# Kernel optimization log

Measured on AMD Instinct MI355X. Metric: run time of the kernel, lower is better.

Reference implementation:

```python
import jax, jax.numpy as jnp
import numpy as np

N_NODES = 50000


def sage_conv(x, src, dst, Wl, bl, Wr):
    # mean-aggregate neighbor features: message from src -> dst
    msg = x[src]                                            # [E, d]
    agg = jax.ops.segment_sum(msg, dst, num_segments=N_NODES)
    deg = jax.ops.segment_sum(jnp.ones((src.shape[0],), x.dtype), dst,
                              num_segments=N_NODES)
    mean = agg / jnp.clip(deg, 1.0)[:, None]                # [N, d]
    # PyG SAGEConv: lin_l(mean) + lin_r(x); lin_l has bias, lin_r does not
    return mean @ Wl.T + bl + x @ Wr.T


def setup_inputs() -> dict:
    key = jax.random.key(0)
    ks = jax.random.split(key, 10)
    d_in, d_h = 128, 256
    E = 800000
    x = jax.random.normal(ks[0], (N_NODES, d_in), jnp.float32)
    edge_index = jax.random.randint(ks[1], (2, E), 0, N_NODES, jnp.int32)
    s = 0.05
    return {
        "x": x,
        "edge_index": edge_index,
        "W1_l": jax.random.normal(ks[2], (d_h, d_in), jnp.float32) * s,
        "b1": jax.random.normal(ks[3], (d_h,), jnp.float32) * s,
        "W1_r": jax.random.normal(ks[4], (d_h, d_in), jnp.float32) * s,
        "W2_l": jax.random.normal(ks[5], (d_h, d_h), jnp.float32) * s,
        "b2": jax.random.normal(ks[6], (d_h,), jnp.float32) * s,
        "W2_r": jax.random.normal(ks[7], (d_h, d_h), jnp.float32) * s,
        "head_w": jax.random.normal(ks[8], (1, d_h), jnp.float32) * s,
        "head_b": jax.random.normal(ks[9], (1,), jnp.float32) * s,
    }


def reference(x, edge_index, W1_l, b1, W1_r, W2_l, b2, W2_r, head_w, head_b):
    src, dst = edge_index[0], edge_index[1]
    h = jax.nn.relu(sage_conv(x, src, dst, W1_l, b1, W1_r))
    # dropout is identity in eval mode
    h = jax.nn.relu(sage_conv(h, src, dst, W2_l, b2, W2_r))
    out = h @ head_w.T + head_b                              # [N, 1]
    return out[:, 0]                                         # [N]
```

## Files before the change

### kernel.cpp

```cpp
#include <hip/hip_runtime.h>
#include <hip/hip_bf16.h>
#include <hip/hip_fp8.h>

#define D_IN 128
#define D_H  256
#define NBLK 128
#define BSH  7
#define BNODES 128
#define MAXCH 6400

typedef __attribute__((ext_vector_type(8))) short short8;
typedef __attribute__((ext_vector_type(4))) float floatx4;
typedef __attribute__((ext_vector_type(4))) unsigned short ushortx4;

__device__ __forceinline__ unsigned short f2bf(float f) {
    __hip_bfloat16 h = __float2bfloat16(f);
    return *reinterpret_cast<unsigned short*>(&h);
}
__device__ __forceinline__ unsigned char f2fp8(float f) {
    __hip_fp8_e4m3 t(f);
    return (unsigned char)t.__x;
}

__device__ __forceinline__ void excl_scan512(int* vals, int NB, int* part) {
    const int t = threadIdx.x;
    const int i0 = t * 2, i1 = t * 2 + 1;
    int v0 = (i0 < NB) ? vals[i0] : 0;
    int v1 = (i1 < NB) ? vals[i1] : 0;
    part[t] = v0 + v1;
    __syncthreads();
    for (int off = 1; off < 256; off <<= 1) {
        int u = (t >= off) ? part[t - off] : 0;
        __syncthreads();
        part[t] += u;
        __syncthreads();
    }
    const int pre = (t == 0) ? 0 : part[t - 1];
    if (i0 < NB) vals[i0] = pre;
    if (i1 < NB) vals[i1] = pre + v0;
    __syncthreads();
}

__global__ void p1_hist_conv_k(const int* __restrict__ dst, int* __restrict__ cnt2d,
                               int E, int NB,
                               const float* __restrict__ x,
                               unsigned char* __restrict__ xb8, int nx4,
                               const float* __restrict__ w1l, unsigned short* __restrict__ w1lb,
                               const float* __restrict__ w1r, unsigned short* __restrict__ w1rb, int nw14,
                               const float* __restrict__ w2l, unsigned short* __restrict__ w2lb,
                               const float* __restrict__ w2r, unsigned short* __restrict__ w2rb, int nw24) {
    if (blockIdx.x < NBLK) {
        __shared__ int h[512];
        for (int i = threadIdx.x; i < NB; i += 256) h[i] = 0;
        __syncthreads();
        const int CH = (E + NBLK - 1) / NBLK;
        const int e0 = blockIdx.x * CH;
        const int e1 = min(e0 + CH, E);
        for (int e = e0 + threadIdx.x; e < e1; e += 256)
            atomicAdd(&h[dst[e] >> BSH], 1);
        __syncthreads();
        for (int i = threadIdx.x; i < NB; i += 256)
            cnt2d[blockIdx.x * NB + i] = h[i];
        return;
    }
    int i = (blockIdx.x - NBLK) * 256 + threadIdx.x;
    if (i < nx4) {
        float4 v = ((const float4*)x)[i];
        uchar4 c;
        c.x = f2fp8(v.x); c.y = f2fp8(v.y); c.z = f2fp8(v.z); c.w = f2fp8(v.w);
        ((uchar4*)xb8)[i] = c;
        return;
    }
    i -= nx4;
    const float* s; unsigned short* d; int k;
    if (i < nw14) { s = w1l; d = w1lb; k = i; }
    else {
        i -= nw14;
        if (i < nw14) { s = w1r; d = w1rb; k = i; }
        else {
            i -= nw14;
            if (i < nw24) { s = w2l; d = w2lb; k = i; }
            else {
                i -= nw24;
                if (i >= nw24) return;
                s = w2r; d = w2rb; k = i;
            }
        }
    }
    float4 v = ((const float4*)s)[k];
    ushort4 u;
    u.x = f2bf(v.x); u.y = f2bf(v.y); u.z = f2bf(v.z); u.w = f2bf(v.w);
    ((ushort4*)d)[k] = u;
}

__global__ __launch_bounds__(NBLK) void bucket_scan_k(const int* __restrict__ cnt2d,
                                                      int* __restrict__ off2d,
                                                      int* __restrict__ tot, int NB) {
    const int B = blockIdx.x, t = threadIdx.x;
    __shared__ int sc[NBLK];
    __shared__ int orig[NBLK];
    int v = cnt2d[t * NB + B];
    orig[t] = v; sc[t] = v;
    __syncthreads();
    for (int off = 1; off < NBLK; off <<= 1) {
        int u = (t >= off) ? sc[t - off] : 0;
        __syncthreads();
        sc[t] += u;
        __syncthreads();
    }
    off2d[t * NB + B] = sc[t] - orig[t];
    if (t == NBLK - 1) tot[B] = sc[t];
}

__global__ __launch_bounds__(256) void place_k(const int* __restrict__ src,
                                               const int* __restrict__ dst,
                                               const int* __restrict__ cnt2d,
                                               const int* __restrict__ off2d,
                                               const int* __restrict__ tot,
                                               unsigned int* __restrict__ staging,
                                               int E, int NB) {
    __shared__ unsigned int lstage[MAXCH];
    __shared__ int lstart[512], lcur[512], runstart[512];
    __shared__ int part[256];
    const int b = blockIdx.x, tid = threadIdx.x;
    const int CH = (E + NBLK - 1) / NBLK;
    const int e0 = b * CH;
    const int e1 = min(e0 + CH, E);
    const int n = e1 - e0;

    for (int i = tid; i < NB; i += 256) {
        lstart[i] = cnt2d[b * NB + i];
        runstart[i] = tot[i];
    }
    __syncthreads();
    excl_scan512(lstart, NB, part);
    excl_scan512(runstart, NB, part);
    for (int i = tid; i < NB; i += 256) {
        runstart[i] += off2d[b * NB + i];
        lcur[i] = lstart[i];
    }
    __syncthreads();
    for (int e = e0 + tid; e < e1; e += 256) {
        const int d = dst[e];
        const int pos = atomicAdd(&lcur[d >> BSH], 1);
        lstage[pos] = ((unsigned int)d << 16) | (unsigned int)src[e];
    }
    __syncthreads();
    for (int i = tid; i < n; i += 256) {
        const unsigned int u = lstage[i];
        const int bkt = (int)(u >> (16 + BSH));
        staging[runstart[bkt] + (i - lstart[bkt])] = u;
    }
}

__global__ __launch_bounds__(256) void bucket_sort_k(const unsigned int* __restrict__ staging,
                                                     const int* __restrict__ tot,
                                                     int* __restrict__ rp, int* __restrict__ col,
                                                     int M, int NB) {
    const int B = blockIdx.x, tid = threadIdx.x;
    __shared__ int red[256];
    __shared__ int h[BNODES], sc[BNODES], cur[BNODES];
    __shared__ int s0s, s1s;
    int acc = 0;
    for (int i = tid; i < B; i += 256) acc += tot[i];
    red[tid] = acc; __syncthreads();
    for (int off = 128; off > 0; off >>= 1) {
        if (tid < off) red[tid] += red[tid + off];
        __syncthreads();
    }
    if (tid == 0) { s0s = red[0]; s1s = red[0] + tot[B]; }
    if (tid < BNODES) h[tid] = 0;
    __syncthreads();
    const int s0 = s0s, s1 = s1s;
    for (int i = s0 + tid; i < s1; i += 256)
        atomicAdd(&h[(staging[i] >> 16) & (BNODES - 1)], 1);
    __syncthreads();
    if (tid < BNODES) sc[tid] = h[tid];
    __syncthreads();
    for (int off = 1; off < BNODES; off <<= 1) {
        int v = 0;
        if (tid < BNODES && tid >= off) v = sc[tid - off];
        __syncthreads();
        if (tid < BNODES) sc[tid] += v;
        __syncthreads();
    }
    if (tid < BNODES) {
        const int excl = sc[tid] - h[tid];
        const int node = B * BNODES + tid;
        if (node < M) rp[node] = s0 + excl;
        cur[tid] = s0 + excl;
    }
    if (B == NB - 1 && tid == 0) rp[M] = s1;
    __syncthreads();
    for (int i = s0 + tid; i < s1; i += 256) {
        const unsigned int u = staging[i];
        const int pos = atomicAdd(&cur[(u >> 16) & (BNODES - 1)], 1);
        col[pos] = (int)(u & 0xFFFFu);
    }
}

template <int UNP>
__device__ __forceinline__ int agg1_stage(const unsigned char* __restrict__ X8,
                                          const int* __restrict__ col,
                                          int j, int e, int sel, int l32, float* acc) {
    for (; j + 2 * UNP <= e; j += 2 * UNP) {
        int c0[UNP], c1[UNP];
#pragma unroll
        for (int u = 0; u < UNP; ++u) {
            c0[u] = __builtin_nontemporal_load(col + j + 2 * u);
            c1[u] = __builtin_nontemporal_load(col + j + 2 * u + 1);
        }
        unsigned int vals[UNP];
#pragma unroll
        for (int u = 0; u < UNP; ++u) {
            const int cs = sel ? c1[u] : c0[u];
            vals[u] = *(const unsigned int*)(X8 + (size_t)cs * 128 + l32 * 4);
        }
#pragma unroll
        for (int u = 0; u < UNP; ++u) {
            __hip_fp8x4_e4m3 p;
            p.__x = vals[u];
            float4 f = (float4)p;
            acc[0] += f.x; acc[1] += f.y; acc[2] += f.z; acc[3] += f.w;
        }
    }
    return j;
}

__global__ __launch_bounds__(256) void aggregate1_k(
    const unsigned char* __restrict__ X8, const int* __restrict__ col,
    const int* __restrict__ rp, unsigned short* __restrict__ out, int Mnodes) {
    int node = __builtin_amdgcn_readfirstlane((blockIdx.x << 2) + (threadIdx.x >> 6));
    if (node >= Mnodes) return;
    const int lane = threadIdx.x & 63;
    const int sel = lane >> 5;
    const int l32 = lane & 31;
    const int s = rp[node], e = rp[node + 1];
    float acc[4] = {0.f, 0.f, 0.f, 0.f};

    int j = s;
    j = agg1_stage<4>(X8, col, j, e, sel, l32, acc);
    j = agg1_stage<2>(X8, col, j, e, sel, l32, acc);
    j = agg1_stage<1>(X8, col, j, e, sel, l32, acc);
    if (j < e) {
        const int c0 = col[j];
        if (sel == 0) {
            unsigned int v = *(const unsigned int*)(X8 + (size_t)c0 * 128 + l32 * 4);
            __hip_fp8x4_e4m3 p;
            p.__x = v;
            float4 f = (float4)p;
            acc[0] += f.x; acc[1] += f.y; acc[2] += f.z; acc[3] += f.w;
        }
    }
#pragma unroll
    for (int k = 0; k < 4; ++k) acc[k] += __shfl_xor(acc[k], 32, 64);
    const float inv = 1.f / fmaxf((float)(e - s), 1.f);
    if (sel == 0) {
        ushortx4 o;
        o.x = f2bf(acc[0] * inv); o.y = f2bf(acc[1] * inv);
        o.z = f2bf(acc[2] * inv); o.w = f2bf(acc[3] * inv);
        __builtin_nontemporal_store(o, (ushortx4*)(out + (size_t)node * 128 + l32 * 4));
    }
}

template <int UN>
__device__ __forceinline__ int agg_stage_fp8(const unsigned char* __restrict__ X8,
                                             const int* __restrict__ col,
                                             int j, int e, int lane, float* acc) {
    for (; j + UN <= e; j += UN) {
        int cs[UN];
#pragma unroll
        for (int u = 0; u < UN; ++u) cs[u] = __builtin_nontemporal_load(col + j + u);
        unsigned int vals[UN];
#pragma unroll
        for (int u = 0; u < UN; ++u)
            vals[u] = *(const unsigned int*)(X8 + (size_t)cs[u] * 256 + lane * 4);
#pragma unroll
        for (int u = 0; u < UN; ++u) {
            __hip_fp8x4_e4m3 p;
            p.__x = vals[u];
            float4 f = (float4)p;
            acc[0] += f.x; acc[1] += f.y; acc[2] += f.z; acc[3] += f.w;
        }
    }
    return j;
}

__global__ __launch_bounds__(256) void aggregate2_k(
    const unsigned char* __restrict__ X8, const int* __restrict__ col,
    const int* __restrict__ rp, unsigned short* __restrict__ out, int Mnodes) {
    int node = __builtin_amdgcn_readfirstlane((blockIdx.x << 2) + (threadIdx.x >> 6));
    if (node >= Mnodes) return;
    const int lane = threadIdx.x & 63;
    const int s = rp[node], e = rp[node + 1];
    float acc[4] = {0.f, 0.f, 0.f, 0.f};

    int j = s;
    j = agg_stage_fp8<8>(X8, col, j, e, lane, acc);
    j = agg_stage_fp8<4>(X8, col, j, e, lane, acc);
    j = agg_stage_fp8<2>(X8, col, j, e, lane, acc);
    j = agg_stage_fp8<1>(X8, col, j, e, lane, acc);

    const float inv = 1.f / fmaxf((float)(e - s), 1.f);
    ushortx4 o;
    o.x = f2bf(acc[0] * inv); o.y = f2bf(acc[1] * inv);
    o.z = f2bf(acc[2] * inv); o.w = f2bf(acc[3] * inv);
    __builtin_nontemporal_store(o, (ushortx4*)(out + (size_t)node * 256 + lane * 4));
}

template <int K, bool HEAD, bool A2F32>
__global__ __launch_bounds__(256, 4) void gemm_mfma_k(
    const unsigned short* __restrict__ A1, const unsigned short* __restrict__ W1,
    const unsigned short* __restrict__ A2, const float* __restrict__ A2f,
    const unsigned short* __restrict__ W2,
    const float* __restrict__ bias, unsigned short* __restrict__ Hout,
    unsigned char* __restrict__ Hout8,
    const float* __restrict__ hw, const float* __restrict__ hb,
    float* __restrict__ out, int M) {
    __shared__ __align__(16) unsigned short sA[64 * 40];
    __shared__ __align__(16) unsigned short sB[256 * 40];
    __shared__ float head_acc[64];

    constexpr int NCK = K / 32;
    constexpr int NC = 2 * NCK;

    const int tid = threadIdx.x;
    const int wave = tid >> 6;
    const int lane = tid & 63;
    const int c = lane & 15;
    const int q = lane >> 4;
    const int m0 = blockIdx.x * 64;

    if (HEAD && tid < 64) head_acc[tid] = 0.f;

    floatx4 acc[4][4];
#pragma unroll
    for (int mi = 0; mi < 4; ++mi)
#pragma unroll
        for (int ni = 0; ni < 4; ++ni) acc[mi][ni] = (floatx4){0.f, 0.f, 0.f, 0.f};

    const int arow = tid >> 2;
    const int aseg = (tid & 3) * 8;
    const int brow = tid >> 2;
    const int bseg = (tid & 3) * 8;
    int gr = m0 + arow;
    if (gr >= M) gr = M - 1;

    auto loadChunk = [&](int t, short8& a0, short8* b) {
        const unsigned short* Wp = (t >= NCK) ? W2 : W1;
        const int k0 = (t & (NCK - 1)) * 32;
        if (A2F32 && t >= NCK) {
            const float* p = A2f + (size_t)gr * K + k0 + aseg;
            float4 u0 = *(const float4*)(p);
            float4 u1 = *(const float4*)(p + 4);
            a0 = (short8){(short)f2bf(u0.x), (short)f2bf(u0.y), (short)f2bf(u0.z), (short)f2bf(u0.w),
                          (short)f2bf(u1.x), (short)f2bf(u1.y), (short)f2bf(u1.z), (short)f2bf(u1.w)};
        } else {
            const unsigned short* Ap = (t >= NCK) ? A2 : A1;
            a0 = *(const short8*)(Ap + (size_t)gr * K + k0 + aseg);
        }
#pragma unroll
        for (int i = 0; i < 4; ++i)
            b[i] = *(const short8*)(Wp + (size_t)(brow + i * 64) * K + k0 + bseg);
    };

    short8 ca0, cb[4], na0, nb[4];
    loadChunk(0, ca0, cb);

#pragma unroll 1
    for (int t = 0; t < NC; ++t) {
        __syncthreads();
        *(short8*)&sA[arow * 40 + aseg] = ca0;
#pragma unroll
        for (int i = 0; i < 4; ++i)
            *(short8*)&sB[(brow + i * 64) * 40 + bseg] = cb[i];
        if (t + 1 < NC)
            loadChunk(t + 1, na0, nb);
        __syncthreads();

        short8 af[4], bf[4];
#pragma unroll
        for (int mi = 0; mi < 4; ++mi)
            af[mi] = *(const short8*)&sA[(mi * 16 + c) * 40 + q * 8];
#pragma unroll
        for (int ni = 0; ni < 4; ++ni)
            bf[ni] = *(const short8*)&sB[(wave * 64 + ni * 16 + c) * 40 + q * 8];
#pragma unroll
        for (int mi = 0; mi < 4; ++mi)
#pragma unroll
            for (int ni = 0; ni < 4; ++ni)
                acc[mi][ni] = __builtin_amdgcn_mfma_f32_16x16x32_bf16(
                    af[mi], bf[ni], acc[mi][ni], 0, 0, 0);

        ca0 = na0;
#pragma unroll
        for (int i = 0; i < 4; ++i) cb[i] = nb[i];
    }

    if (!HEAD) {
#pragma unroll
        for (int mi = 0; mi < 4; ++mi)
#pragma unroll
            for (int ni = 0; ni < 4; ++ni) {
                const int n = wave * 64 + ni * 16 + c;
                const float bv = bias[n];
#pragma unroll
                for (int reg = 0; reg < 4; ++reg) {
                    const int m = m0 + mi * 16 + q * 4 + reg;
                    if (m < M) {
                        float v = fmaxf(acc[mi][ni][reg] + bv, 0.f);
                        __builtin_nontemporal_store(f2bf(v), &Hout[(size_t)m * 256 + n]);
                        Hout8[(size_t)m * 256 + n] = f2fp8(v);
                    }
                }
            }
    } else {
#pragma unroll
        for (int mi = 0; mi < 4; ++mi) {
            float p[4] = {0.f, 0.f, 0.f, 0.f};
#pragma unroll
            for (int ni = 0; ni < 4; ++ni) {
                const int n = wave * 64 + ni * 16 + c;
                const float bv = bias[n];
                const float hv = hw[n];
#pragma unroll
                for (int reg = 0; reg < 4; ++reg)
                    p[reg] += fmaxf(acc[mi][ni][reg] + bv, 0.f) * hv;
            }
#pragma unroll
            for (int reg = 0; reg < 4; ++reg) {
                float v = p[reg];
                v += __shfl_xor(v, 1, 64);
                v += __shfl_xor(v, 2, 64);
                v += __shfl_xor(v, 4, 64);
                v += __shfl_xor(v, 8, 64);
                if (c == 0) atomicAdd(&head_acc[mi * 16 + q * 4 + reg], v);
            }
        }
        __syncthreads();
        if (tid < 64) {
            const int m = m0 + tid;
            if (m < M) out[m] = head_acc[tid] + hb[0];
        }
    }
}

extern "C" void kernel_launch(void* const* d_in, const int* in_sizes, int n_in,
                              void* d_out, int out_size, void* d_ws, size_t ws_size,
                              hipStream_t stream) {
    const float* x    = (const float*)d_in[0];
    const int*   ei   = (const int*)d_in[1];
    const float* W1l  = (const float*)d_in[2];
    const float* b1   = (const float*)d_in[3];
    const float* W1r  = (const float*)d_in[4];
    const float* W2l  = (const float*)d_in[5];
    const float* b2   = (const float*)d_in[6];
    const float* W2r  = (const float*)d_in[7];
    const float* hw   = (const float*)d_in[8];
    const float* hb   = (const float*)d_in[9];
    float* out = (float*)d_out;

    const int M = in_sizes[0] / D_IN;
    const int E = in_sizes[1] / 2;
    const int* src = ei;
    const int* dst = ei + E;
    const int NB = (M + BNODES - 1) / BNODES;

    size_t off = 0;
    auto alloc = [&](size_t bytes) -> void* {
        void* p = (char*)d_ws + off;
        off += (bytes + 255) & ~(size_t)255;
        return p;
    };
    int* cnt2d = (int*)alloc((size_t)NBLK * NB * 4);
    int* off2d = (int*)alloc((size_t)NBLK * NB * 4);
    int* tot   = (int*)alloc((size_t)NB * 4);
    unsigned int* staging = (unsigned int*)alloc((size_t)E * 4);
    int* rp    = (int*)alloc((size_t)(M + 1) * 4);
    int* col   = (int*)alloc((size_t)E * 4);
    unsigned char*  xb8   = (unsigned char*)alloc((size_t)M * D_IN);
    unsigned short* w1lb  = (unsigned short*)alloc((size_t)D_H * D_IN * 2);
    unsigned short* w1rb  = (unsigned short*)alloc((size_t)D_H * D_IN * 2);
    unsigned short* w2lb  = (unsigned short*)alloc((size_t)D_H * D_H * 2);
    unsigned short* w2rb  = (unsigned short*)alloc((size_t)D_H * D_H * 2);
    unsigned short* mean1 = (unsigned short*)alloc((size_t)M * D_IN * 2);
    unsigned short* h1    = (unsigned short*)alloc((size_t)M * D_H * 2);
    unsigned char*  h8    = (unsigned char*)alloc((size_t)M * D_H);
    unsigned short* mean2 = (unsigned short*)alloc((size_t)M * D_H * 2);

    const int nx4 = (M * D_IN) / 4;
    const int nw14 = (D_H * D_IN) / 4;
    const int nw24 = (D_H * D_H) / 4;
    const int tot4 = nx4 + 2 * nw14 + 2 * nw24;
    const int convblk = (tot4 + 255) / 256;
    p1_hist_conv_k<<<NBLK + convblk, 256, 0, stream>>>(
        dst, cnt2d, E, NB,
        x, xb8, nx4, W1l, w1lb, W1r, w1rb, nw14, W2l, w2lb, W2r, w2rb, nw24);
    bucket_scan_k<<<NB, NBLK, 0, stream>>>(cnt2d, off2d, tot, NB);
    place_k<<<NBLK, 256, 0, stream>>>(src, dst, cnt2d, off2d, tot, staging, E, NB);
    bucket_sort_k<<<NB, 256, 0, stream>>>(staging, tot, rp, col, M, NB);

    const int nblk = (M + 63) / 64;
    const int ablk = (M + 3) / 4;

    aggregate1_k<<<ablk, 256, 0, stream>>>(xb8, col, rp, mean1, M);
    gemm_mfma_k<D_IN, false, true><<<nblk, 256, 0, stream>>>(
        mean1, w1lb, nullptr, x, w1rb, b1, h1, h8, nullptr, nullptr, nullptr, M);

    aggregate2_k<<<ablk, 256, 0, stream>>>(h8, col, rp, mean2, M);
    gemm_mfma_k<D_H, true, false><<<nblk, 256, 0, stream>>>(
        mean2, w2lb, h1, nullptr, w2rb, b2, nullptr, nullptr, hw, hb, out, M);
}
```

Before: 240.3 us.

## Fuse neighbor mean aggregation into GEMM kernels via shared-memory mean tile

Removes the separate aggregate kernels and computes each 64-node tile's neighbor mean directly into shared memory inside the GEMM kernel, which now runs with 512 threads (8 waves, each covering 32 output columns). This avoids writing and re-reading the bf16 mean1/mean2 buffers through global memory and saves two kernel launches. The cost is a serial gather phase at the start of each GEMM block (8 nodes per wave) with no overlap with the MFMA work, a larger shared-memory footprint, and only about 782 blocks to hide gather latency, so occupancy may limit it.

```diff
diff --git a/kernel.cpp b/kernel.cpp
--- a/kernel.cpp
+++ b/kernel.cpp
@@ -227,42 +227,6 @@
     return j;
 }
 
-__global__ __launch_bounds__(256) void aggregate1_k(
-    const unsigned char* __restrict__ X8, const int* __restrict__ col,
-    const int* __restrict__ rp, unsigned short* __restrict__ out, int Mnodes) {
-    int node = __builtin_amdgcn_readfirstlane((blockIdx.x << 2) + (threadIdx.x >> 6));
-    if (node >= Mnodes) return;
-    const int lane = threadIdx.x & 63;
-    const int sel = lane >> 5;
-    const int l32 = lane & 31;
-    const int s = rp[node], e = rp[node + 1];
-    float acc[4] = {0.f, 0.f, 0.f, 0.f};
-
-    int j = s;
-    j = agg1_stage<4>(X8, col, j, e, sel, l32, acc);
-    j = agg1_stage<2>(X8, col, j, e, sel, l32, acc);
-    j = agg1_stage<1>(X8, col, j, e, sel, l32, acc);
-    if (j < e) {
-        const int c0 = col[j];
-        if (sel == 0) {
-            unsigned int v = *(const unsigned int*)(X8 + (size_t)c0 * 128 + l32 * 4);
-            __hip_fp8x4_e4m3 p;
-            p.__x = v;
-            float4 f = (float4)p;
-            acc[0] += f.x; acc[1] += f.y; acc[2] += f.z; acc[3] += f.w;
-        }
-    }
-#pragma unroll
-    for (int k = 0; k < 4; ++k) acc[k] += __shfl_xor(acc[k], 32, 64);
-    const float inv = 1.f / fmaxf((float)(e - s), 1.f);
-    if (sel == 0) {
-        ushortx4 o;
-        o.x = f2bf(acc[0] * inv); o.y = f2bf(acc[1] * inv);
-        o.z = f2bf(acc[2] * inv); o.w = f2bf(acc[3] * inv);
-        __builtin_nontemporal_store(o, (ushortx4*)(out + (size_t)node * 128 + l32 * 4));
-    }
-}
-
 template <int UN>
 __device__ __forceinline__ int agg_stage_fp8(const unsigned char* __restrict__ X8,
                                              const int* __restrict__ col,
@@ -286,39 +250,22 @@
     return j;
 }
 
-__global__ __launch_bounds__(256) void aggregate2_k(
+template <int K, bool HEAD, bool A2F32>
+__global__ __launch_bounds__(512, 4) void gemm_fused_k(
     const unsigned char* __restrict__ X8, const int* __restrict__ col,
-    const int* __restrict__ rp, unsigned short* __restrict__ out, int Mnodes) {
-    int node = __builtin_amdgcn_readfirstlane((blockIdx.x << 2) + (threadIdx.x >> 6));
-    if (node >= Mnodes) return;
-    const int lane = threadIdx.x & 63;
-    const int s = rp[node], e = rp[node + 1];
-    float acc[4] = {0.f, 0.f, 0.f, 0.f};
-
-    int j = s;
-    j = agg_stage_fp8<8>(X8, col, j, e, lane, acc);
-    j = agg_stage_fp8<4>(X8, col, j, e, lane, acc);
-    j = agg_stage_fp8<2>(X8, col, j, e, lane, acc);
-    j = agg_stage_fp8<1>(X8, col, j, e, lane, acc);
-
-    const float inv = 1.f / fmaxf((float)(e - s), 1.f);
-    ushortx4 o;
-    o.x = f2bf(acc[0] * inv); o.y = f2bf(acc[1] * inv);
-    o.z = f2bf(acc[2] * inv); o.w = f2bf(acc[3] * inv);
-    __builtin_nontemporal_store(o, (ushortx4*)(out + (size_t)node * 256 + lane * 4));
-}
-
-template <int K, bool HEAD, bool A2F32>
-__global__ __launch_bounds__(256, 4) void gemm_mfma_k(
-    const unsigned short* __restrict__ A1, const unsigned short* __restrict__ W1,
-    const unsigned short* __restrict__ A2, const float* __restrict__ A2f,
+    const int* __restrict__ rp,
+    const unsigned short* __restrict__ W1,
+    const float* __restrict__ A2f, const unsigned short* __restrict__ A2,
     const unsigned short* __restrict__ W2,
     const float* __restrict__ bias, unsigned short* __restrict__ Hout,
     unsigned char* __restrict__ Hout8,
     const float* __restrict__ hw, const float* __restrict__ hb,
     float* __restrict__ out, int M) {
+
+    constexpr int SMS = K + 8;
+    __shared__ __align__(16) unsigned short sMean[64 * SMS];
+    __shared__ __align__(16) unsigned short sB[256 * 40];
     __shared__ __align__(16) unsigned short sA[64 * 40];
-    __shared__ __align__(16) unsigned short sB[256 * 40];
     __shared__ float head_acc[64];
 
     constexpr int NCK = K / 32;
@@ -333,76 +280,130 @@
 
     if (HEAD && tid < 64) head_acc[tid] = 0.f;
 
-    floatx4 acc[4][4];
+    const int sel = lane >> 5;
+    const int l32 = lane & 31;
+#pragma unroll 1
+    for (int nn = 0; nn < 8; ++nn) {
+        const int lrow = wave * 8 + nn;
+        const int node = m0 + lrow;
+        if (node < M) {
+            const int s = rp[node], e = rp[node + 1];
+            float acc[4] = {0.f, 0.f, 0.f, 0.f};
+            const float inv = 1.f / fmaxf((float)(e - s), 1.f);
+            if (K == 256) {
+                int j = s;
+                j = agg_stage_fp8<8>(X8, col, j, e, lane, acc);
+                j = agg_stage_fp8<4>(X8, col, j, e, lane, acc);
+                j = agg_stage_fp8<2>(X8, col, j, e, lane, acc);
+                j = agg_stage_fp8<1>(X8, col, j, e, lane, acc);
+                ushortx4 o;
+                o.x = f2bf(acc[0] * inv); o.y = f2bf(acc[1] * inv);
+                o.z = f2bf(acc[2] * inv); o.w = f2bf(acc[3] * inv);
+                *(ushortx4*)&sMean[lrow * SMS + lane * 4] = o;
+            } else {
+                int j = s;
+                j = agg1_stage<4>(X8, col, j, e, sel, l32, acc);
+                j = agg1_stage<2>(X8, col, j, e, sel, l32, acc);
+                j = agg1_stage<1>(X8, col, j, e, sel, l32, acc);
+                if (j < e && sel == 0) {
+                    unsigned int v = *(const unsigned int*)(X8 + (size_t)col[j] * 128 + l32 * 4);
+                    __hip_fp8x4_e4m3 p;
+                    p.__x = v;
+                    float4 f = (float4)p;
+                    acc[0] += f.x; acc[1] += f.y; acc[2] += f.z; acc[3] += f.w;
+                }
+#pragma unroll
+                for (int k = 0; k < 4; ++k) acc[k] += __shfl_xor(acc[k], 32, 64);
+                if (sel == 0) {
+                    ushortx4 o;
+                    o.x = f2bf(acc[0] * inv); o.y = f2bf(acc[1] * inv);
+                    o.z = f2bf(acc[2] * inv); o.w = f2bf(acc[3] * inv);
+                    *(ushortx4*)&sMean[lrow * SMS + l32 * 4] = o;
+                }
+            }
+        } else {
+            if (K == 256) {
+                *(ushortx4*)&sMean[lrow * SMS + lane * 4] = (ushortx4){0, 0, 0, 0};
+            } else if (sel == 0) {
+                *(ushortx4*)&sMean[lrow * SMS + l32 * 4] = (ushortx4){0, 0, 0, 0};
+            }
+        }
+    }
+
+    floatx4 acc[4][2];
 #pragma unroll
     for (int mi = 0; mi < 4; ++mi)
 #pragma unroll
-        for (int ni = 0; ni < 4; ++ni) acc[mi][ni] = (floatx4){0.f, 0.f, 0.f, 0.f};
-
-    const int arow = tid >> 2;
-    const int aseg = (tid & 3) * 8;
-    const int brow = tid >> 2;
-    const int bseg = (tid & 3) * 8;
+        for (int ni = 0; ni < 2; ++ni) acc[mi][ni] = (floatx4){0.f, 0.f, 0.f, 0.f};
+
+    const int brow = tid >> 1;
+    const int bseg = (tid & 1) * 16;
+    const int arow = tid >> 3;
+    const int aseg = (tid & 7) * 4;
     int gr = m0 + arow;
     if (gr >= M) gr = M - 1;
 
-    auto loadChunk = [&](int t, short8& a0, short8* b) {
+    auto loadChunk = [&](int t, ushortx4& a0, short8* b) {
         const unsigned short* Wp = (t >= NCK) ? W2 : W1;
         const int k0 = (t & (NCK - 1)) * 32;
-        if (A2F32 && t >= NCK) {
-            const float* p = A2f + (size_t)gr * K + k0 + aseg;
-            float4 u0 = *(const float4*)(p);
-            float4 u1 = *(const float4*)(p + 4);
-            a0 = (short8){(short)f2bf(u0.x), (short)f2bf(u0.y), (short)f2bf(u0.z), (short)f2bf(u0.w),
-                          (short)f2bf(u1.x), (short)f2bf(u1.y), (short)f2bf(u1.z), (short)f2bf(u1.w)};
-        } else {
-            const unsigned short* Ap = (t >= NCK) ? A2 : A1;
-            a0 = *(const short8*)(Ap + (size_t)gr * K + k0 + aseg);
-        }
-#pragma unroll
-        for (int i = 0; i < 4; ++i)
-            b[i] = *(const short8*)(Wp + (size_t)(brow + i * 64) * K + k0 + bseg);
+        if (t >= NCK) {
+            if (A2F32) {
+                float4 u = *(const float4*)(A2f + (size_t)gr * K + k0 + aseg);
+                a0.x = f2bf(u.x); a0.y = f2bf(u.y); a0.z = f2bf(u.z); a0.w = f2bf(u.w);
+            } else {
+                a0 = *(const ushortx4*)(A2 + (size_t)gr * K + k0 + aseg);
+            }
+        }
+        b[0] = *(const short8*)(Wp + (size_t)brow * K + k0 + bseg);
+        b[1] = *(const short8*)(Wp + (size_t)brow * K + k0 + bseg + 8);
     };
 
-    short8 ca0, cb[4], na0, nb[4];
+    ushortx4 ca0, na0;
+    short8 cb[2], nb[2];
     loadChunk(0, ca0, cb);
 
 #pragma unroll 1
     for (int t = 0; t < NC; ++t) {
         __syncthreads();
-        *(short8*)&sA[arow * 40 + aseg] = ca0;
-#pragma unroll
-        for (int i = 0; i < 4; ++i)
-            *(short8*)&sB[(brow + i * 64) * 40 + bseg] = cb[i];
+        if (t >= NCK)
+            *(ushortx4*)&sA[arow * 40 + aseg] = ca0;
+        *(short8*)&sB[brow * 40 + bseg] = cb[0];
+        *(short8*)&sB[brow * 40 + bseg + 8] = cb[1];
         if (t + 1 < NC)
             loadChunk(t + 1, na0, nb);
         __syncthreads();
 
-        short8 af[4], bf[4];
+        short8 af[4], bf[2];
+        if (t < NCK) {
+            const int k0 = t * 32;
+#pragma unroll
+            for (int mi = 0; mi < 4; ++mi)
+                af[mi] = *(const short8*)&sMean[(mi * 16 + c) * SMS + k0 + q * 8];
+        } else {
+#pragma unroll
+            for (int mi = 0; mi < 4; ++mi)
+                af[mi] = *(const short8*)&sA[(mi * 16 + c) * 40 + q * 8];
+        }
+#pragma unroll
+        for (int ni = 0; ni < 2; ++ni)
+            bf[ni] = *(const short8*)&sB[(wave * 32 + ni * 16 + c) * 40 + q * 8];
 #pragma unroll
         for (int mi = 0; mi < 4; ++mi)
-            af[mi] = *(const short8*)&sA[(mi * 16 + c) * 40 + q * 8];
-#pragma unroll
-        for (int ni = 0; ni < 4; ++ni)
-            bf[ni] = *(const short8*)&sB[(wave * 64 + ni * 16 + c) * 40 + q * 8];
-#pragma unroll
-        for (int mi = 0; mi < 4; ++mi)
-#pragma unroll
-            for (int ni = 0; ni < 4; ++ni)
+#pragma unroll
+            for (int ni = 0; ni < 2; ++ni)
                 acc[mi][ni] = __builtin_amdgcn_mfma_f32_16x16x32_bf16(
                     af[mi], bf[ni], acc[mi][ni], 0, 0, 0);
 
         ca0 = na0;
-#pragma unroll
-        for (int i = 0; i < 4; ++i) cb[i] = nb[i];
+        cb[0] = nb[0]; cb[1] = nb[1];
     }
 
     if (!HEAD) {
 #pragma unroll
         for (int mi = 0; mi < 4; ++mi)
 #pragma unroll
-            for (int ni = 0; ni < 4; ++ni) {
-                const int n = wave * 64 + ni * 16 + c;
+            for (int ni = 0; ni < 2; ++ni) {
+                const int n = wave * 32 + ni * 16 + c;
                 const float bv = bias[n];
 #pragma unroll
                 for (int reg = 0; reg < 4; ++reg) {
@@ -419,8 +420,8 @@
         for (int mi = 0; mi < 4; ++mi) {
             float p[4] = {0.f, 0.f, 0.f, 0.f};
 #pragma unroll
-            for (int ni = 0; ni < 4; ++ni) {
-                const int n = wave * 64 + ni * 16 + c;
+            for (int ni = 0; ni < 2; ++ni) {
+                const int n = wave * 32 + ni * 16 + c;
                 const float bv = bias[n];
                 const float hv = hw[n];
 #pragma unroll
@@ -483,10 +484,8 @@
     unsigned short* w1rb  = (unsigned short*)alloc((size_t)D_H * D_IN * 2);
     unsigned short* w2lb  = (unsigned short*)alloc((size_t)D_H * D_H * 2);
     unsigned short* w2rb  = (unsigned short*)alloc((size_t)D_H * D_H * 2);
-    unsigned short* mean1 = (unsigned short*)alloc((size_t)M * D_IN * 2);
     unsigned short* h1    = (unsigned short*)alloc((size_t)M * D_H * 2);
     unsigned char*  h8    = (unsigned char*)alloc((size_t)M * D_H);
-    unsigned short* mean2 = (unsigned short*)alloc((size_t)M * D_H * 2);
 
     const int nx4 = (M * D_IN) / 4;
     const int nw14 = (D_H * D_IN) / 4;
@@ -501,13 +500,12 @@
     bucket_sort_k<<<NB, 256, 0, stream>>>(staging, tot, rp, col, M, NB);
 
     const int nblk = (M + 63) / 64;
-    const int ablk = (M + 3) / 4;
-
-    aggregate1_k<<<ablk, 256, 0, stream>>>(xb8, col, rp, mean1, M);
-    gemm_mfma_k<D_IN, false, true><<<nblk, 256, 0, stream>>>(
-        mean1, w1lb, nullptr, x, w1rb, b1, h1, h8, nullptr, nullptr, nullptr, M);
-
-    aggregate2_k<<<ablk, 256, 0, stream>>>(h8, col, rp, mean2, M);
-    gemm_mfma_k<D_H, true, false><<<nblk, 256, 0, stream>>>(
-        mean2, w2lb, h1, nullptr, w2rb, b2, nullptr, nullptr, hw, hb, out, M);
-}
+
+    gemm_fused_k<D_IN, false, true><<<nblk, 512, 0, stream>>>(
+        xb8, col, rp, w1lb, x, nullptr, w1rb, b1, h1, h8,
+        nullptr, nullptr, nullptr, M);
+
+    gemm_fused_k<D_H, true, false><<<nblk, 512, 0, stream>>>(
+        h8, col, rp, w2lb, nullptr, h1, w2rb, b2, nullptr, nullptr,
+        hw, hb, out, M);
+}
```

Result: slower. 296.5 us (+23.4%).
